# Kernel optimization log

Measured on AMD Instinct MI355X. Metric: run time of the kernel, lower is better.

## Reference

```python
import jax, jax.numpy as jnp
import numpy as np

N = 131072   # nodes
E = 2097152  # edges (avg degree 16)
B = 4096     # subgraph (center) nodes, ntype == -1
D = 64       # feature dim (in_nfeats == all latent dims)
L = 3        # number of (local, global) RelGraphConv pairs
R = 3        # num relations
NB = 2       # num bases


def setup_inputs() -> dict:
    key = jax.random.key(0)
    ks = jax.random.split(key, 20)
    s = 0.05
    return {
        "x": jax.random.normal(ks[0], (N, D), jnp.float32),
        "src": jax.random.randint(ks[1], (E,), 0, N, jnp.int32),
        "dst": jax.random.randint(ks[2], (E,), 0, N, jnp.int32),
        "etype": jax.random.randint(ks[3], (E,), 0, R, jnp.int32),
        "mask": jax.random.uniform(ks[4], (E,), jnp.float32),
        "mask2": jax.random.uniform(ks[5], (E,), jnp.float32),
        # local RelGraphConv params (basis decomposition): W_r = sum_b C[r,b] * V[b]
        "lV": jax.random.normal(ks[6], (L, NB, D, D), jnp.float32) * s,
        "lC": jax.random.normal(ks[7], (L, R, NB), jnp.float32),
        "lW": jax.random.normal(ks[8], (L, D, D), jnp.float32) * s,   # self-loop weight
        "lB": jnp.zeros((L, D), jnp.float32),
        # global RelGraphConv params
        "gV": jax.random.normal(ks[9], (L, NB, D, D), jnp.float32) * s,
        "gC": jax.random.normal(ks[10], (L, R, NB), jnp.float32),
        "gW": jax.random.normal(ks[11], (L, D, D), jnp.float32) * s,
        "gB": jnp.zeros((L, D), jnp.float32),
        # MLP head: lin1 (sum(latent_dim)=192 -> 128), lin2 (128 -> 1)
        "w1": jax.random.normal(ks[12], (128, L * D), jnp.float32) * s,
        "b1": jnp.zeros((128,), jnp.float32),
        "w2": jax.random.normal(ks[13], (1, 128), jnp.float32) * s,
        "b2": jnp.zeros((1,), jnp.float32),
        "num_subg": B,
    }


def _rel_graph_conv(h, V, C, W, b, src, dst, etype, norm):
    """Basis-decomposed RelGraphConv with self-loop (DGL semantics, eval mode)."""
    n = h.shape[0]
    hV = jnp.einsum('nd,bdo->nbo', h, V)                  # [N, NB, D]
    coef = C[etype]                                        # [E, NB] edge-type gather
    msg = jnp.einsum('eb,ebo->eo', coef, hV[src])          # [E, D]
    msg = msg * norm[:, None]                              # per-edge norm (edge_mask)
    agg = jax.ops.segment_sum(msg, dst, num_segments=n)    # scatter-add to dst
    return agg + h @ W + b                                 # + self-loop + bias


def reference(x, src, dst, etype, mask, mask2, lV, lC, lW, lB,
              gV, gC, gW, gB, w1, b1, w2, b2, num_subg):
    # eval mode: edge_drop and Dropout(0.5) are identity
    h = x
    subg_states = []
    for i in range(L):
        h = jax.nn.elu(_rel_graph_conv(h, lV[i], lC[i], lW[i], lB[i],
                                       src, dst, etype, mask))
        # (ui_states collected in original but unused for 'center' embedding)
        h = jax.nn.leaky_relu(_rel_graph_conv(h, gV[i], gC[i], gW[i], gB[i],
                                              src, dst, etype, mask2),
                              negative_slope=0.01)
        subg_states.append(h)
    subg = jnp.concatenate(subg_states, axis=1)[:num_subg]  # subgraph-center nodes
    hid = jnp.maximum(subg @ w1.T + b1, 0.0)
    out = jax.nn.sigmoid(hid @ w2.T + b2)
    return out[:, 0]
```

## Files before the change

### kernel.cpp

```cpp
#include <hip/hip_runtime.h>
#include <math.h>

#define N_NODES 131072
#define N_EDGES 2097152
#define DIM     64
#define BSUB    4096
#define NREL    3
#define NBASES  2
#define NCB     512
#define CBSZ    8192

typedef unsigned short u16;
typedef __attribute__((ext_vector_type(8))) short bf16x8;
typedef __attribute__((ext_vector_type(4))) float f32x4;

__device__ __forceinline__ float bf2f(u16 x) {
    return __uint_as_float(((unsigned)x) << 16);
}
__device__ __forceinline__ u16 f2bf(float f) {
    unsigned u = __float_as_uint(f);
    unsigned r = (u + 0x7FFFu + ((u >> 16) & 1u)) >> 16;
    return (u16)r;
}
__device__ __forceinline__ float4 bf4_to_f4(ushort4 u) {
    return make_float4(bf2f(u.x), bf2f(u.y), bf2f(u.z), bf2f(u.w));
}
__device__ __forceinline__ ushort4 f4_to_bf4(float4 v) {
    ushort4 o; o.x = f2bf(v.x); o.y = f2bf(v.y); o.z = f2bf(v.z); o.w = f2bf(v.w);
    return o;
}


__global__ void initmark_kernel(int* __restrict__ mark, int* __restrict__ chist) {
    int i = blockIdx.x * 256 + threadIdx.x;
    if (i < N_NODES) mark[i] = (i < BSUB) ? 1 : 0;
    if (i < NCB) chist[i] = 0;
}

__global__ __launch_bounds__(256) void chist_kernel(const int* __restrict__ dst,
                                                    int* __restrict__ chist) {
    __shared__ int lh[NCB];
    int tid = threadIdx.x;
    lh[tid] = 0; lh[tid + 256] = 0;
    __syncthreads();
    int base = blockIdx.x * CBSZ;
#pragma unroll
    for (int j = 0; j < CBSZ / 1024; j++) {
        int4 d4 = *(const int4*)(dst + base + j * 1024 + tid * 4);
        atomicAdd(&lh[d4.x >> 8], 1);
        atomicAdd(&lh[d4.y >> 8], 1);
        atomicAdd(&lh[d4.z >> 8], 1);
        atomicAdd(&lh[d4.w >> 8], 1);
    }
    __syncthreads();
    atomicAdd(&chist[tid], lh[tid]);
    atomicAdd(&chist[tid + 256], lh[tid + 256]);
}

__global__ void cscan_kernel(const int* __restrict__ chist, int* __restrict__ cbase,
                             int* __restrict__ ccur, int* __restrict__ offs) {
    __shared__ int s[NCB];
    int tid = threadIdx.x;
    int v = chist[tid];
    s[tid] = v;
    __syncthreads();
    int val = v;
    for (int off = 1; off < NCB; off <<= 1) {
        int tmp = (tid >= off) ? s[tid - off] : 0;
        __syncthreads();
        val += tmp;
        s[tid] = val;
        __syncthreads();
    }
    cbase[tid] = val - v;
    ccur[tid] = val - v;
    if (tid == 0) offs[N_NODES] = N_EDGES;
}

__global__ __launch_bounds__(512) void cscatter_kernel(
    const int* __restrict__ src, const int* __restrict__ dst,
    const int* __restrict__ et, const float* __restrict__ m1,
    const float* __restrict__ m2, int* __restrict__ ccur,
    int4* __restrict__ tmp, int* __restrict__ mark) {
    __shared__ int lh[NCB];
    __shared__ int lbase[NCB];
    int tid = threadIdx.x;
    lh[tid] = 0;
    __syncthreads();
    int e0b = blockIdx.x * CBSZ;
#pragma unroll
    for (int j = 0; j < CBSZ / 2048; j++) {
        int4 d4 = *(const int4*)(dst + e0b + j * 2048 + tid * 4);
        atomicAdd(&lh[d4.x >> 8], 1);
        atomicAdd(&lh[d4.y >> 8], 1);
        atomicAdd(&lh[d4.z >> 8], 1);
        atomicAdd(&lh[d4.w >> 8], 1);
    }
    __syncthreads();
    int c = lh[tid];
    lbase[tid] = c ? atomicAdd(&ccur[tid], c) : 0;
    lh[tid] = 0;
    __syncthreads();
#pragma unroll
    for (int j = 0; j < CBSZ / 2048; j++) {
        int e0 = e0b + j * 2048 + tid * 4;
        int4  d4 = *(const int4*)(dst + e0);
        int4  s4 = *(const int4*)(src + e0);
        int4  t4 = *(const int4*)(et + e0);
        float4 a4 = *(const float4*)(m1 + e0);
        float4 b4 = *(const float4*)(m2 + e0);
#pragma unroll
        for (int k = 0; k < 4; k++) {
            int d = (&d4.x)[k];
            int s = (&s4.x)[k];
            int b = d >> 8;
            int r = atomicAdd(&lh[b], 1);
            int4 v;
            v.x = s | ((&t4.x)[k] << 20);
            v.y = __float_as_int((&a4.x)[k]);
            v.z = __float_as_int((&b4.x)[k]);
            v.w = d;
            tmp[lbase[b] + r] = v;
            if (d < BSUB) mark[s] = 1;
        }
    }
}

__global__ __launch_bounds__(256) void fscatter_kernel(
    const int4* __restrict__ tmp, const int* __restrict__ cbase,
    const int* __restrict__ chist, int* __restrict__ offs,
    int4* __restrict__ csr) {
    __shared__ int lh[256];
    __shared__ int lpre[256];
    __shared__ int s[256];
    int b = blockIdx.x;
    int tid = threadIdx.x;
    int base = cbase[b], cnt = chist[b];
    lh[tid] = 0;
    __syncthreads();
    int i = 0;
    for (; i + 1024 <= cnt; i += 1024) {
        int4 v0 = tmp[base + i + tid * 4 + 0];
        int4 v1 = tmp[base + i + tid * 4 + 1];
        int4 v2 = tmp[base + i + tid * 4 + 2];
        int4 v3 = tmp[base + i + tid * 4 + 3];
        atomicAdd(&lh[v0.w & 255], 1);
        atomicAdd(&lh[v1.w & 255], 1);
        atomicAdd(&lh[v2.w & 255], 1);
        atomicAdd(&lh[v3.w & 255], 1);
    }
    for (int k = i + tid; k < cnt; k += 256)
        atomicAdd(&lh[tmp[base + k].w & 255], 1);
    __syncthreads();
    int v = lh[tid];
    s[tid] = v;
    __syncthreads();
    int val = v;
    for (int off = 1; off < 256; off <<= 1) {
        int tq = (tid >= off) ? s[tid - off] : 0;
        __syncthreads();
        val += tq;
        s[tid] = val;
        __syncthreads();
    }
    int ex = val - v;
    lpre[tid] = ex;
    offs[b * 256 + tid] = base + ex;
    lh[tid] = 0;
    __syncthreads();
    i = 0;
    for (; i + 1024 <= cnt; i += 1024) {
        int4 v0 = tmp[base + i + tid * 4 + 0];
        int4 v1 = tmp[base + i + tid * 4 + 1];
        int4 v2 = tmp[base + i + tid * 4 + 2];
        int4 v3 = tmp[base + i + tid * 4 + 3];
        int k0 = v0.w & 255; int r0 = atomicAdd(&lh[k0], 1); csr[base + lpre[k0] + r0] = v0;
        int k1 = v1.w & 255; int r1 = atomicAdd(&lh[k1], 1); csr[base + lpre[k1] + r1] = v1;
        int k2 = v2.w & 255; int r2 = atomicAdd(&lh[k2], 1); csr[base + lpre[k2] + r2] = v2;
        int k3 = v3.w & 255; int r3 = atomicAdd(&lh[k3], 1); csr[base + lpre[k3] + r3] = v3;
    }
    for (int kk = i + tid; kk < cnt; kk += 256) {
        int4 vv = tmp[base + kk];
        int k = vv.w & 255;
        int r = atomicAdd(&lh[k], 1);
        csr[base + lpre[k] + r] = vv;
    }
}

__global__ void scan1_kernel(const int* __restrict__ cnt, int* __restrict__ scanned,
                             int* __restrict__ bsum) {
    __shared__ int s[256];
    int tid = threadIdx.x;
    int i = blockIdx.x * 256 + tid;
    int v = cnt[i];
    s[tid] = v;
    __syncthreads();
    int val = v;
    for (int off = 1; off < 256; off <<= 1) {
        int tmp = (tid >= off) ? s[tid - off] : 0;
        __syncthreads();
        val += tmp;
        s[tid] = val;
        __syncthreads();
    }
    scanned[i] = val - v;
    if (tid == 255) bsum[blockIdx.x] = val;
}

__global__ void scan2_kernel(int* __restrict__ bsum) {
    __shared__ int s[512];
    int tid = threadIdx.x;
    int v = bsum[tid];
    s[tid] = v;
    __syncthreads();
    int val = v;
    for (int off = 1; off < 512; off <<= 1) {
        int tmp = (tid >= off) ? s[tid - off] : 0;
        __syncthreads();
        val += tmp;
        s[tid] = val;
        __syncthreads();
    }
    bsum[tid] = val - v;
}

__global__ void listfill_kernel(const int* __restrict__ mark, const int* __restrict__ mpref,
                                const int* __restrict__ mbsum, int* __restrict__ list,
                                int* __restrict__ nld) {
    int i = blockIdx.x * 256 + threadIdx.x;
    int pos = mpref[i] + mbsum[blockIdx.x];
    if (mark[i]) list[pos] = i;
    if (i == N_NODES - 1) *nld = pos + mark[i];
}

__global__ void cvt_kernel(const float4* __restrict__ x, ushort4* __restrict__ hb, int n4) {
    int i = blockIdx.x * 256 + threadIdx.x;
    if (i < n4) hb[i] = f4_to_bf4(x[i]);
}

__global__ void wpack_kernel(const float* __restrict__ lV, const float* __restrict__ lW,
                             const float* __restrict__ gV, const float* __restrict__ gW,
                             u16* __restrict__ wfrag) {
    int idx = blockIdx.x * 256 + threadIdx.x;
    if (idx >= 6 * 4 * 6 * 64) return;
    int lane = idx & 63;
    int kidx = (idx >> 6) % 6;
    int nt   = (idx >> 6) / 6 % 4;
    int c    = idx / (64 * 6 * 4);
    int layer = c >> 1;
    bool isglobal = c & 1;
    const float* V = isglobal ? gV : lV;
    const float* W = isglobal ? gW : lW;
    int n = nt * 16 + (lane & 15);
    int kbase = kidx * 32 + (lane >> 4) * 8;
    u16 vals[8];
#pragma unroll
    for (int j = 0; j < 8; j++) {
        int r = kbase + j;
        float val;
        if (r < NBASES * DIM) {
            int b = r >> 6, d = r & 63;
            val = V[((layer * NBASES + b) * DIM + d) * DIM + n];
        } else {
            int d = r - NBASES * DIM;
            val = W[(layer * DIM + d) * DIM + n];
        }
        vals[j] = f2bf(val);
    }
    ushort4* o = (ushort4*)(wfrag + (size_t)idx * 8);
    o[0] = make_ushort4(vals[0], vals[1], vals[2], vals[3]);
    o[1] = make_ushort4(vals[4], vals[5], vals[6], vals[7]);
}

__global__ __launch_bounds__(256) void aggmm_kernel(
    const ushort4* __restrict__ hb, const int* __restrict__ offs,
    const int4* __restrict__ csr, const float* __restrict__ Cc,
    int which, const u16* __restrict__ wfrag, const float* __restrict__ bias,
    u16* __restrict__ hout, float* __restrict__ subg, int subg_off, int act,
    int nNodes, const int* __restrict__ list, const int* __restrict__ nld) {
    __shared__ int4 lmeta[4][64];
    __shared__ alignas(16) ushort4 t_tile[16][34];
    int lane = threadIdx.x & 63;
    int wid  = threadIdx.x >> 6;
    int q  = lane >> 4;
    int ql = lane & 15;
    int nld_v = list ? *nld : 0;
    int slot0 = blockIdx.x << 4;
    if (list && slot0 >= nld_v) return;
    float Ca0 = Cc[0], Cb0 = Cc[1], Ca1 = Cc[2], Cb1 = Cc[3], Ca2 = Cc[4], Cb2 = Cc[5];

    for (int i = 0; i < 4; i++) {
        int slot = slot0 + (wid << 2) + i;
        int n = -1;
        if (list) { if (slot < nld_v) n = list[slot]; }
        else if (slot < nNodes) n = slot;
        float4 a0 = make_float4(0.f, 0.f, 0.f, 0.f);
        float4 a1 = make_float4(0.f, 0.f, 0.f, 0.f);
        if (n >= 0) {
            int beg = offs[n], end = offs[n + 1];
            for (int base = beg; base < end; base += 64) {
                int cnt = min(64, end - base);
                int pp = 0; float c0 = 0.f, c1 = 0.f;
                if (lane < cnt) {
                    int4 meta = csr[base + lane];
                    int et = ((unsigned)meta.x) >> 20;
                    float m = __int_as_float(which ? meta.z : meta.y);
                    float ca = et == 0 ? Ca0 : (et == 1 ? Ca1 : Ca2);
                    float cb = et == 0 ? Cb0 : (et == 1 ? Cb1 : Cb2);
                    pp = (meta.x & 0xFFFFF) << 4;
                    c0 = m * ca;
                    c1 = m * cb;
                }
                lmeta[wid][lane] = make_int4(pp, __float_as_int(c0), __float_as_int(c1), 0);
                for (int j = 0; j < cnt; j += 16) {
#pragma unroll
                    for (int s = 0; s < 4; s++) {
                        int4 md = lmeta[wid][j + (s << 2) + q];
                        ushort4 rv = hb[md.x + ql];
                        float4 v = bf4_to_f4(rv);
                        float e0 = __int_as_float(md.y);
                        float e1 = __int_as_float(md.z);
                        a0.x = fmaf(e0, v.x, a0.x); a0.y = fmaf(e0, v.y, a0.y);
                        a0.z = fmaf(e0, v.z, a0.z); a0.w = fmaf(e0, v.w, a0.w);
                        a1.x = fmaf(e1, v.x, a1.x); a1.y = fmaf(e1, v.y, a1.y);
                        a1.z = fmaf(e1, v.z, a1.z); a1.w = fmaf(e1, v.w, a1.w);
                    }
                }
            }
#pragma unroll
            for (int off = 16; off < 64; off <<= 1) {
                a0.x += __shfl_xor(a0.x, off, 64); a0.y += __shfl_xor(a0.y, off, 64);
                a0.z += __shfl_xor(a0.z, off, 64); a0.w += __shfl_xor(a0.w, off, 64);
                a1.x += __shfl_xor(a1.x, off, 64); a1.y += __shfl_xor(a1.y, off, 64);
                a1.z += __shfl_xor(a1.z, off, 64); a1.w += __shfl_xor(a1.w, off, 64);
            }
            if (q < 2)
                t_tile[(wid << 2) + i][(q << 4) + ql] = f4_to_bf4(q == 0 ? a0 : a1);
        }
    }
    __syncthreads();

    int l16 = ql;
    int quad = q;
    int myslot = slot0 + l16;
    int rowA = list ? list[min(myslot, nld_v - 1)] : min(myslot, nNodes - 1);
    const u16* hrow = (const u16*)hb + (size_t)rowA * 64;
    const u16* trow = (const u16*)&t_tile[l16][0];
    f32x4 acc = {0.f, 0.f, 0.f, 0.f};
#pragma unroll
    for (int kidx = 0; kidx < 6; kidx++) {
        bf16x8 a = (kidx < 4)
            ? *(const bf16x8*)(trow + kidx * 32 + quad * 8)
            : *(const bf16x8*)(hrow + (kidx - 4) * 32 + quad * 8);
        bf16x8 b = *(const bf16x8*)(wfrag + ((size_t)(wid * 6 + kidx) * 64 + lane) * 8);
        acc = __builtin_amdgcn_mfma_f32_16x16x32_bf16(a, b, acc, 0, 0, 0);
    }
    int col = wid * 16 + l16;
    float bcol = bias[col];
#pragma unroll
    for (int r = 0; r < 4; r++) {
        int cslot = slot0 + quad * 4 + r;
        if (list && cslot >= nld_v) continue;
        int row = list ? __shfl(rowA, quad * 4 + r, 64) : cslot;
        float xv = acc[r] + bcol;
        float v = act ? (xv > 0.f ? xv : 0.01f * xv)
                      : (xv > 0.f ? xv : expm1f(xv));
        hout[(size_t)row * 64 + col] = f2bf(v);
        if (subg && row < BSUB)
            subg[(size_t)row * 192 + subg_off + col] = v;
    }
}

__global__ __launch_bounds__(256) void head_kernel(
    const float* __restrict__ subg, const float* __restrict__ w1,
    const float* __restrict__ b1, const float* __restrict__ w2,
    const float* __restrict__ b2, float* __restrict__ out) {
    __shared__ float srow[4][192];
    int lane = threadIdx.x & 63, wid = threadIdx.x >> 6;
    int row = blockIdx.x * 4 + wid;
    const float* sr = subg + (size_t)row * 192;
    srow[wid][lane] = sr[lane];
    srow[wid][64 + lane] = sr[64 + lane];
    srow[wid][128 + lane] = sr[128 + lane];
    __syncthreads();
    float acc1 = b1[lane], acc2 = b1[64 + lane];
    const float* w1a = w1 + lane * 192;
    const float* w1b = w1 + (64 + lane) * 192;
    for (int k = 0; k < 192; k++) {
        float s = srow[wid][k];
        acc1 = fmaf(s, w1a[k], acc1);
        acc2 = fmaf(s, w1b[k], acc2);
    }
    acc1 = fmaxf(acc1, 0.f);
    acc2 = fmaxf(acc2, 0.f);
    float part = acc1 * w2[lane] + acc2 * w2[64 + lane];
    for (int off = 32; off; off >>= 1) part += __shfl_down(part, off, 64);
    if (lane == 0) out[row] = 1.f / (1.f + expf(-(part + b2[0])));
}

extern "C" void kernel_launch(void* const* d_in, const int* in_sizes, int n_in,
                              void* d_out, int out_size, void* d_ws, size_t ws_size,
                              hipStream_t stream) {
    const float* x     = (const float*)d_in[0];
    const int*   src   = (const int*)d_in[1];
    const int*   dst   = (const int*)d_in[2];
    const int*   etype = (const int*)d_in[3];
    const float* mask  = (const float*)d_in[4];
    const float* mask2 = (const float*)d_in[5];
    const float* lV = (const float*)d_in[6];
    const float* lC = (const float*)d_in[7];
    const float* lW = (const float*)d_in[8];
    const float* lB = (const float*)d_in[9];
    const float* gV = (const float*)d_in[10];
    const float* gC = (const float*)d_in[11];
    const float* gW = (const float*)d_in[12];
    const float* gB = (const float*)d_in[13];
    const float* w1 = (const float*)d_in[14];
    const float* b1 = (const float*)d_in[15];
    const float* w2 = (const float*)d_in[16];
    const float* b2 = (const float*)d_in[17];
    float* out = (float*)d_out;

    char* ws = (char*)d_ws;
    size_t off = 0;
    auto alloc = [&](size_t bytes) {
        void* p = ws + off;
        off += (bytes + 255) & ~(size_t)255;
        return p;
    };
    ushort4* h0   = (ushort4*)alloc((size_t)N_NODES * 64 * 2);
    ushort4* h1   = (ushort4*)alloc((size_t)N_NODES * 64 * 2);
    int4*  csr    = (int4*)alloc((size_t)N_EDGES * 16);
    int*   offs   = (int*)alloc((size_t)(N_NODES + 1) * 4);
    int*   chist  = (int*)alloc(NCB * 4);
    int*   cbase  = (int*)alloc(NCB * 4);
    int*   ccur   = (int*)alloc(NCB * 4);
    int*   bsum   = (int*)alloc(512 * 4);
    int*   mark   = (int*)alloc((size_t)N_NODES * 4);
    int*   mpref  = (int*)alloc((size_t)N_NODES * 4);
    int*   mbsum  = (int*)alloc(512 * 4);
    int*   list   = (int*)alloc((size_t)N_NODES * 4);
    int*   nld    = (int*)alloc(256);
    u16*   wfrag  = (u16*)alloc((size_t)6 * 4 * 6 * 64 * 8 * 2);
    float* subg   = (float*)alloc((size_t)BSUB * 192 * 4);
    int4*  tmp    = (int4*)h0;

    initmark_kernel<<<N_NODES / 256, 256, 0, stream>>>(mark, chist);
    chist_kernel<<<N_EDGES / CBSZ, 256, 0, stream>>>(dst, chist);
    cscan_kernel<<<1, NCB, 0, stream>>>(chist, cbase, ccur, offs);
    cscatter_kernel<<<N_EDGES / CBSZ, 512, 0, stream>>>(src, dst, etype, mask, mask2,
                                                        ccur, tmp, mark);
    fscatter_kernel<<<NCB, 256, 0, stream>>>(tmp, cbase, chist, offs, csr);
    scan1_kernel<<<N_NODES / 256, 256, 0, stream>>>(mark, mpref, mbsum);
    scan2_kernel<<<1, 512, 0, stream>>>(mbsum);
    listfill_kernel<<<N_NODES / 256, 256, 0, stream>>>(mark, mpref, mbsum, list, nld);
    wpack_kernel<<<(6 * 4 * 6 * 64 + 255) / 256, 256, 0, stream>>>(lV, lW, gV, gW, wfrag);
    cvt_kernel<<<(N_NODES * 64 / 4) / 256, 256, 0, stream>>>((const float4*)x, h0,
                                                             N_NODES * 64 / 4);

    const int convfrag = 4 * 6 * 64 * 8;
    ushort4* hb[2] = {h0, h1};
    int cur = 0;
    for (int layer = 0; layer < 3; layer++) {
        const int* ll = (layer == 2) ? list : nullptr;
        aggmm_kernel<<<N_NODES / 16, 256, 0, stream>>>(
            hb[cur], offs, csr, lC + layer * NREL * NBASES, 0,
            wfrag + (size_t)(layer * 2 + 0) * convfrag, lB + layer * 64,
            (u16*)hb[cur ^ 1], nullptr, 0, 0, N_NODES, ll, nld);
        cur ^= 1;
        int nG = (layer == 2) ? BSUB : N_NODES;
        aggmm_kernel<<<nG / 16, 256, 0, stream>>>(
            hb[cur], offs, csr, gC + layer * NREL * NBASES, 1,
            wfrag + (size_t)(layer * 2 + 1) * convfrag, gB + layer * 64,
            (u16*)hb[cur ^ 1], subg, layer * 64, 1, nG, nullptr, nld);
        cur ^= 1;
    }
    head_kernel<<<BSUB / 4, 256, 0, stream>>>(subg, w1, b1, w2, b2, out);
}
```

Before: 557.0 us.

## Split CSR edge records into per-mask int2 arrays and prefetch next node's metadata

The 16-byte CSR edge record is split into two 8-byte arrays, one per conv type, each holding packed src/etype plus that conv's mask. This halves the metadata bytes each aggregation kernel reads. The aggregation kernel also hoists the offsets for its four nodes and prefetches the next node's first metadata chunk while the current node's neighbours are being gathered, to hide that load's latency. The cost is an extra write stream in fscatter and higher register pressure in the aggregation kernel.

Result: no change. 563.7 us (+1.2%).

```diff
diff --git a/kernel.cpp b/kernel.cpp
--- a/kernel.cpp
+++ b/kernel.cpp
@@ -129,7 +129,7 @@
 __global__ __launch_bounds__(256) void fscatter_kernel(
     const int4* __restrict__ tmp, const int* __restrict__ cbase,
     const int* __restrict__ chist, int* __restrict__ offs,
-    int4* __restrict__ csr) {
+    int2* __restrict__ csr1, int2* __restrict__ csr2) {
     __shared__ int lh[256];
     __shared__ int lpre[256];
     __shared__ int s[256];
@@ -170,20 +170,23 @@
     __syncthreads();
     i = 0;
     for (; i + 1024 <= cnt; i += 1024) {
-        int4 v0 = tmp[base + i + tid * 4 + 0];
-        int4 v1 = tmp[base + i + tid * 4 + 1];
-        int4 v2 = tmp[base + i + tid * 4 + 2];
-        int4 v3 = tmp[base + i + tid * 4 + 3];
-        int k0 = v0.w & 255; int r0 = atomicAdd(&lh[k0], 1); csr[base + lpre[k0] + r0] = v0;
-        int k1 = v1.w & 255; int r1 = atomicAdd(&lh[k1], 1); csr[base + lpre[k1] + r1] = v1;
-        int k2 = v2.w & 255; int r2 = atomicAdd(&lh[k2], 1); csr[base + lpre[k2] + r2] = v2;
-        int k3 = v3.w & 255; int r3 = atomicAdd(&lh[k3], 1); csr[base + lpre[k3] + r3] = v3;
+#pragma unroll
+        for (int u = 0; u < 4; u++) {
+            int4 vv = tmp[base + i + tid * 4 + u];
+            int k = vv.w & 255;
+            int r = atomicAdd(&lh[k], 1);
+            int p = base + lpre[k] + r;
+            csr1[p] = make_int2(vv.x, vv.y);
+            csr2[p] = make_int2(vv.x, vv.z);
+        }
     }
     for (int kk = i + tid; kk < cnt; kk += 256) {
         int4 vv = tmp[base + kk];
         int k = vv.w & 255;
         int r = atomicAdd(&lh[k], 1);
-        csr[base + lpre[k] + r] = vv;
+        int p = base + lpre[k] + r;
+        csr1[p] = make_int2(vv.x, vv.y);
+        csr2[p] = make_int2(vv.x, vv.z);
     }
 }
 
@@ -274,8 +277,8 @@
 
 __global__ __launch_bounds__(256) void aggmm_kernel(
     const ushort4* __restrict__ hb, const int* __restrict__ offs,
-    const int4* __restrict__ csr, const float* __restrict__ Cc,
-    int which, const u16* __restrict__ wfrag, const float* __restrict__ bias,
+    const int2* __restrict__ cs, const float* __restrict__ Cc,
+    const u16* __restrict__ wfrag, const float* __restrict__ bias,
     u16* __restrict__ hout, float* __restrict__ subg, int subg_off, int act,
     int nNodes, const int* __restrict__ list, const int* __restrict__ nld) {
     __shared__ int4 lmeta[4][64];
@@ -289,30 +292,79 @@
     if (list && slot0 >= nld_v) return;
     float Ca0 = Cc[0], Cb0 = Cc[1], Ca1 = Cc[2], Cb1 = Cc[3], Ca2 = Cc[4], Cb2 = Cc[5];
 
+    int nn[4], bg[4], en[4];
+#pragma unroll
     for (int i = 0; i < 4; i++) {
         int slot = slot0 + (wid << 2) + i;
         int n = -1;
         if (list) { if (slot < nld_v) n = list[slot]; }
         else if (slot < nNodes) n = slot;
+        nn[i] = n;
+        bg[i] = (n >= 0) ? offs[n] : 0;
+        en[i] = (n >= 0) ? offs[n + 1] : 0;
+    }
+
+    int2 pref = make_int2(0, 0);
+    if (nn[0] >= 0 && lane < min(64, en[0] - bg[0]))
+        pref = cs[bg[0] + lane];
+
+#pragma unroll
+    for (int i = 0; i < 4; i++) {
+        int n = nn[i];
+        int beg = bg[i], end = en[i];
+        int cnt = min(64, end - beg);
         float4 a0 = make_float4(0.f, 0.f, 0.f, 0.f);
         float4 a1 = make_float4(0.f, 0.f, 0.f, 0.f);
+        {
+            int pp = 0; float c0 = 0.f, c1 = 0.f;
+            if (n >= 0 && lane < cnt) {
+                int mx = pref.x;
+                int et = ((unsigned)mx) >> 20;
+                float m = __int_as_float(pref.y);
+                float ca = et == 0 ? Ca0 : (et == 1 ? Ca1 : Ca2);
+                float cb = et == 0 ? Cb0 : (et == 1 ? Cb1 : Cb2);
+                pp = (mx & 0xFFFFF) << 4;
+                c0 = m * ca;
+                c1 = m * cb;
+            }
+            lmeta[wid][lane] = make_int4(pp, __float_as_int(c0), __float_as_int(c1), 0);
+        }
+        if (i < 3) {
+            int2 nxt = make_int2(0, 0);
+            if (nn[i + 1] >= 0 && lane < min(64, en[i + 1] - bg[i + 1]))
+                nxt = cs[bg[i + 1] + lane];
+            pref = nxt;
+        }
         if (n >= 0) {
-            int beg = offs[n], end = offs[n + 1];
-            for (int base = beg; base < end; base += 64) {
-                int cnt = min(64, end - base);
+            for (int j = 0; j < cnt; j += 16) {
+#pragma unroll
+                for (int s = 0; s < 4; s++) {
+                    int4 md = lmeta[wid][j + (s << 2) + q];
+                    ushort4 rv = hb[md.x + ql];
+                    float4 v = bf4_to_f4(rv);
+                    float e0 = __int_as_float(md.y);
+                    float e1 = __int_as_float(md.z);
+                    a0.x = fmaf(e0, v.x, a0.x); a0.y = fmaf(e0, v.y, a0.y);
+                    a0.z = fmaf(e0, v.z, a0.z); a0.w = fmaf(e0, v.w, a0.w);
+                    a1.x = fmaf(e1, v.x, a1.x); a1.y = fmaf(e1, v.y, a1.y);
+                    a1.z = fmaf(e1, v.z, a1.z); a1.w = fmaf(e1, v.w, a1.w);
+                }
+            }
+            for (int base = beg + 64; base < end; base += 64) {
+                int cc = min(64, end - base);
                 int pp = 0; float c0 = 0.f, c1 = 0.f;
-                if (lane < cnt) {
-                    int4 meta = csr[base + lane];
-                    int et = ((unsigned)meta.x) >> 20;
-                    float m = __int_as_float(which ? meta.z : meta.y);
+                if (lane < cc) {
+                    int2 mm = cs[base + lane];
+                    int et = ((unsigned)mm.x) >> 20;
+                    float m = __int_as_float(mm.y);
                     float ca = et == 0 ? Ca0 : (et == 1 ? Ca1 : Ca2);
                     float cb = et == 0 ? Cb0 : (et == 1 ? Cb1 : Cb2);
-                    pp = (meta.x & 0xFFFFF) << 4;
+                    pp = (mm.x & 0xFFFFF) << 4;
                     c0 = m * ca;
                     c1 = m * cb;
                 }
                 lmeta[wid][lane] = make_int4(pp, __float_as_int(c0), __float_as_int(c1), 0);
-                for (int j = 0; j < cnt; j += 16) {
+                for (int j = 0; j < cc; j += 16) {
 #pragma unroll
                     for (int s = 0; s < 4; s++) {
                         int4 md = lmeta[wid][j + (s << 2) + q];
@@ -430,7 +482,8 @@
     };
     ushort4* h0   = (ushort4*)alloc((size_t)N_NODES * 64 * 2);
     ushort4* h1   = (ushort4*)alloc((size_t)N_NODES * 64 * 2);
-    int4*  csr    = (int4*)alloc((size_t)N_EDGES * 16);
+    int2*  csr1   = (int2*)alloc((size_t)N_EDGES * 8);
+    int2*  csr2   = (int2*)alloc((size_t)N_EDGES * 8);
     int*   offs   = (int*)alloc((size_t)(N_NODES + 1) * 4);
     int*   chist  = (int*)alloc(NCB * 4);
     int*   cbase  = (int*)alloc(NCB * 4);
@@ -450,7 +503,7 @@
     cscan_kernel<<<1, NCB, 0, stream>>>(chist, cbase, ccur, offs);
     cscatter_kernel<<<N_EDGES / CBSZ, 512, 0, stream>>>(src, dst, etype, mask, mask2,
                                                         ccur, tmp, mark);
-    fscatter_kernel<<<NCB, 256, 0, stream>>>(tmp, cbase, chist, offs, csr);
+    fscatter_kernel<<<NCB, 256, 0, stream>>>(tmp, cbase, chist, offs, csr1, csr2);
     scan1_kernel<<<N_NODES / 256, 256, 0, stream>>>(mark, mpref, mbsum);
     scan2_kernel<<<1, 512, 0, stream>>>(mbsum);
     listfill_kernel<<<N_NODES / 256, 256, 0, stream>>>(mark, mpref, mbsum, list, nld);
@@ -464,13 +517,13 @@
     for (int layer = 0; layer < 3; layer++) {
         const int* ll = (layer == 2) ? list : nullptr;
         aggmm_kernel<<<N_NODES / 16, 256, 0, stream>>>(
-            hb[cur], offs, csr, lC + layer * NREL * NBASES, 0,
+            hb[cur], offs, csr1, lC + layer * NREL * NBASES,
             wfrag + (size_t)(layer * 2 + 0) * convfrag, lB + layer * 64,
             (u16*)hb[cur ^ 1], nullptr, 0, 0, N_NODES, ll, nld);
         cur ^= 1;
         int nG = (layer == 2) ? BSUB : N_NODES;
         aggmm_kernel<<<nG / 16, 256, 0, stream>>>(
-            hb[cur], offs, csr, gC + layer * NREL * NBASES, 1,
+            hb[cur], offs, csr2, gC + layer * NREL * NBASES,
             wfrag + (size_t)(layer * 2 + 1) * convfrag, gB + layer * 64,
             (u16*)hb[cur ^ 1], subg, layer * 64, 1, nG, nullptr, nld);
         cur ^= 1;
```
